# Kernel tuning notes

Measured on AMD Instinct MI355X. Metric: run time of the kernel, lower is better.

Reference implementation:

```python
import jax, jax.numpy as jnp
import numpy as np

B, S, D_MODEL, H = 4, 1024, 1024, 16
HD = D_MODEL // H  # head_dim = 64


def setup_inputs() -> dict:
    key = jax.random.key(0)
    ks = jax.random.split(key, 12)
    sd = 1.0 / np.sqrt(D_MODEL)
    return {
        "x": jax.random.normal(ks[0], (B, S, D_MODEL), dtype=jnp.float32),
        "Wq": jax.random.normal(ks[1], (D_MODEL, D_MODEL), dtype=jnp.float32) * sd,
        "bq": jnp.zeros((D_MODEL,), dtype=jnp.float32),
        "Wk": jax.random.normal(ks[2], (D_MODEL, D_MODEL), dtype=jnp.float32) * sd,
        "bk": jnp.zeros((D_MODEL,), dtype=jnp.float32),
        "Wv": jax.random.normal(ks[3], (D_MODEL, D_MODEL), dtype=jnp.float32) * sd,
        "bv": jnp.zeros((D_MODEL,), dtype=jnp.float32),
        "W1": jax.random.normal(ks[4], (2 * D_MODEL, D_MODEL), dtype=jnp.float32) * sd,
        "b1": jnp.zeros((2 * D_MODEL,), dtype=jnp.float32),
        "W2": jax.random.normal(ks[5], (D_MODEL, 2 * D_MODEL), dtype=jnp.float32) * (1.0 / np.sqrt(2 * D_MODEL)),
        "b2": jnp.zeros((D_MODEL,), dtype=jnp.float32),
        "mask": jnp.ones((B, S, S), dtype=jnp.int32),
    }


def reference(x, Wq, bq, Wk, bk, Wv, bv, W1, b1, W2, b2, mask):
    # QKV projections (torch Linear: y = x @ W.T + b), split into heads -> [B,H,S,HD]
    def proj(W, b):
        return (x @ W.T + b).reshape(B, S, H, HD).transpose(0, 2, 1, 3)

    q = proj(Wq, bq)
    k = proj(Wk, bk)
    v = proj(Wv, bv)

    scores = jnp.einsum("bhqd,bhkd->bhqk", q, k) / jnp.sqrt(jnp.float32(HD))
    # mask [B,S,S] broadcast over heads (original does unsqueeze(1).repeat)
    scores = jnp.where(mask[:, None, :, :] == 0, jnp.float32(-1e8), scores)
    probs = jax.nn.softmax(scores, axis=-1)
    ctx = jnp.einsum("bhqk,bhkd->bhqd", probs, v)
    ctx = ctx.transpose(0, 2, 1, 3).reshape(B, S, D_MODEL)

    # out-projection MLP: Linear(d, 2d) -> ReLU -> Linear(2d, d)
    h = jax.nn.relu(ctx @ W1.T + b1)
    return h @ W2.T + b2
```

## Files before the change

kernel.cpp:

```cpp
#include <hip/hip_runtime.h>
#include <hip/hip_bf16.h>
#include <stdint.h>


#define B_ 4
#define S_ 1024
#define DM_ 1024
#define H_ 16
#define HD_ 64

typedef __attribute__((ext_vector_type(8))) short short8;
typedef __attribute__((ext_vector_type(4))) float f32x4;
typedef __attribute__((ext_vector_type(4))) unsigned short ushort4v;

#define GLB_AS(p) ((const __attribute__((address_space(1))) void*)(p))
#define LDS_AS(p) ((__attribute__((address_space(3))) void*)(p))

__device__ __forceinline__ void async_load16(const void* g, void* l) {
  __builtin_amdgcn_global_load_lds(GLB_AS(g), LDS_AS(l), 16, 0, 0);
}

__device__ __forceinline__ unsigned short f2bf(float x) {
  union { float f; unsigned int u; } v; v.f = x;
  unsigned int r = v.u + 0x7fffu + ((v.u >> 16) & 1u);
  return (unsigned short)(r >> 16);
}

#define QSCALE 0.18033688011112042f

struct PrepArgs {
  const float* src[6];
  unsigned short* dst[6];
  int n4[6];
  const int* mask;
  unsigned long long* bits;
  unsigned int* rowflag;
  const float* bq;
  const float* bk;
  const float* bv;
  float* cb;
};

__global__ void prep_kernel(PrepArgs a) {
  const int seg = blockIdx.y;
  if (seg < 6) {
    const int n4 = a.n4[seg];
    const f32x4* __restrict__ src = (const f32x4*)a.src[seg];
    ushort4v* __restrict__ dst = (ushort4v*)a.dst[seg];
    for (int i = blockIdx.x * blockDim.x + threadIdx.x; i < n4;
         i += gridDim.x * blockDim.x) {
      f32x4 v = src[i];
      ushort4v o;
      o[0] = f2bf(v[0]); o[1] = f2bf(v[1]); o[2] = f2bf(v[2]); o[3] = f2bf(v[3]);
      dst[i] = o;
    }
  } else if (seg == 6) {
    const int wave = threadIdx.x >> 6;
    const int lane = threadIdx.x & 63;
    const int row = blockIdx.x * 4 + wave;
    const int4* mr = (const int4*)(a.mask + (size_t)row * S_) + lane * 4;
    unsigned int chunk = 0;
#pragma unroll
    for (int t = 0; t < 4; ++t) {
      const int4 v = mr[t];
      chunk |= (v.x != 0 ? 1u : 0u) << (4 * t + 0);
      chunk |= (v.y != 0 ? 1u : 0u) << (4 * t + 1);
      chunk |= (v.z != 0 ? 1u : 0u) << (4 * t + 2);
      chunk |= (v.w != 0 ? 1u : 0u) << (4 * t + 3);
    }
    unsigned long long v64 = (unsigned long long)chunk << (16 * (lane & 3));
    v64 |= __shfl_xor(v64, 1);
    v64 |= __shfl_xor(v64, 2);
    if ((lane & 3) == 0) a.bits[(size_t)row * 16 + (lane >> 2)] = v64;
    const bool all1 = (__ballot(chunk == 0xffffu) == ~0ull);
    if (lane == 0) a.rowflag[row] = all1 ? 1u : 0u;
  } else {
    const int i = blockIdx.x * 256 + threadIdx.x;
    if (i < 3072) {
      const float* src = (i < 1024) ? a.bq : (i < 2048) ? a.bk : a.bv;
      a.cb[i] = src[i & 1023];
    }
  }
}

enum { EPI_QKV = 0, EPI_RELU_BF16 = 2 };

template <int EPI>
__global__ __launch_bounds__(256, 3) void gemm_bt(
    const unsigned short* __restrict__ A, const unsigned short* __restrict__ Bt,
    const float* __restrict__ bias, void* __restrict__ Cp,
    unsigned short* __restrict__ Vt, int M, int N, int K, int Kld) {
  __shared__ __align__(16) unsigned short smem[128 * 136];
  unsigned short* sA = smem;
  unsigned short* sB = smem + 128 * 64;

  const int tid = threadIdx.x;
  const int lane = tid & 63;
  const int wave = tid >> 6;
  const int quad = lane >> 4;
  const int l15 = lane & 15;
  const int swzb = l15 & 7;
  const int m0 = blockIdx.y * 128;
  const int n0 = blockIdx.x * 128;
  const int wm = (wave >> 1) * 64;
  const int wn = (wave & 1) * 64;

  f32x4 acc[4][4];
#pragma unroll
  for (int i = 0; i < 4; ++i)
#pragma unroll
    for (int j = 0; j < 4; ++j) acc[i][j] = (f32x4){0.f, 0.f, 0.f, 0.f};

  const int srow = tid >> 3;
  const int scol = ((tid & 7) ^ (srow & 7)) * 8;
  const unsigned short* gA = A + (size_t)(m0 + srow) * Kld + scol;
  const unsigned short* gB = Bt + (size_t)(n0 + srow) * Kld + scol;
  unsigned short* lA = sA + tid * 8;
  unsigned short* lB = sB + tid * 8;

  for (int k0 = 0; k0 < K; k0 += 64) {
    __syncthreads();
#pragma unroll
    for (int st = 0; st < 4; ++st) {
      async_load16(gA + (size_t)(st * 32) * Kld + k0, lA + st * 2048);
      async_load16(gB + (size_t)(st * 32) * Kld + k0, lB + st * 2048);
    }
    __syncthreads();

#pragma unroll
    for (int ks = 0; ks < 2; ++ks) {
      short8 af[4], bfr[4];
#pragma unroll
      for (int t = 0; t < 4; ++t) {
        const int cg = ((ks * 4 + quad) ^ swzb) * 8;
        af[t] = *(const short8*)(sA + (wm + t * 16 + l15) * 64 + cg);
        bfr[t] = *(const short8*)(sB + (wn + t * 16 + l15) * 64 + cg);
      }
#pragma unroll
      for (int mt = 0; mt < 4; ++mt)
#pragma unroll
        for (int nt = 0; nt < 4; ++nt)
          acc[mt][nt] = __builtin_amdgcn_mfma_f32_16x16x32_bf16(
              af[mt], bfr[nt], acc[mt][nt], 0, 0, 0);
    }
  }

  if (EPI == EPI_QKV && n0 >= 2048) {
    __syncthreads();
#pragma unroll
    for (int nt = 0; nt < 4; ++nt) {
      const int col = n0 + wn + nt * 16 + l15;
      const float bv = bias[col];
#pragma unroll
      for (int mt = 0; mt < 4; ++mt)
#pragma unroll
        for (int r = 0; r < 4; ++r)
          smem[(wn + nt * 16 + l15) * 136 + wm + mt * 16 + quad * 4 + r] =
              f2bf(acc[mt][nt][r] + bv);
    }
    __syncthreads();
    const int vc0 = n0 - 2048;
    const int bb = m0 >> 10;
    const int s0 = m0 & 1023;
#pragma unroll
    for (int i = 0; i < 8; ++i) {
      const int c = i * 16 + (tid >> 4);
      const int tc = tid & 15;
      const short8 val = *(const short8*)(smem + c * 136 + tc * 8);
      const int ch = vc0 + c;
      const int hh = ch >> 6, dd = ch & 63;
      *(short8*)(Vt + ((size_t)(bb * 16 + hh) * HD_ + dd) * S_ + s0 + tc * 8) =
          val;
    }
    return;
  }

#pragma unroll
  for (int nt = 0; nt < 4; ++nt) {
    const int col = n0 + wn + nt * 16 + l15;
    const float bv = bias[col];
    const float scl = (EPI == EPI_QKV && col < 1024) ? QSCALE : 1.0f;
#pragma unroll
    for (int mt = 0; mt < 4; ++mt) {
#pragma unroll
      for (int r = 0; r < 4; ++r) {
        const int row = m0 + wm + mt * 16 + quad * 4 + r;
        float v = acc[mt][nt][r] + bv;
        if (EPI == EPI_RELU_BF16) {
          ((unsigned short*)Cp)[(size_t)row * N + col] = f2bf(fmaxf(v, 0.f));
        } else {
          ((unsigned short*)Cp)[(size_t)row * N + col] = f2bf(v * scl);
        }
      }
    }
  }
}

__global__ __launch_bounds__(512, 1) void gemm_ffn2(
    const unsigned short* __restrict__ A, const unsigned short* __restrict__ Bt,
    const float* __restrict__ bias, float* __restrict__ out) {
  __shared__ __align__(16) unsigned short smem[4 * 128 * 64];
  const int tid512 = threadIdx.x;
  const int half = tid512 >> 8;
  const int tid = tid512 & 255;
  unsigned short* sA = smem + half * 2 * 128 * 64;
  unsigned short* sB = sA + 128 * 64;

  const int lane = tid & 63;
  const int wave = tid >> 6;
  const int quad = lane >> 4;
  const int l15 = lane & 15;
  const int swzb = l15 & 7;
  const int m0 = blockIdx.y * 128;
  const int n0 = blockIdx.x * 128;
  const int wm = (wave >> 1) * 64;
  const int wn = (wave & 1) * 64;
  const int kz = half * 1024;

  f32x4 acc[4][4];
#pragma unroll
  for (int i = 0; i < 4; ++i)
#pragma unroll
    for (int j = 0; j < 4; ++j) acc[i][j] = (f32x4){0.f, 0.f, 0.f, 0.f};

  const int srow = tid >> 3;
  const int scol = ((tid & 7) ^ (srow & 7)) * 8;
  const unsigned short* gA = A + (size_t)(m0 + srow) * 2048 + kz + scol;
  const unsigned short* gB = Bt + (size_t)(n0 + srow) * 2048 + kz + scol;
  unsigned short* lA = sA + tid * 8;
  unsigned short* lB = sB + tid * 8;

  for (int k0 = 0; k0 < 1024; k0 += 64) {
    __syncthreads();
#pragma unroll
    for (int st = 0; st < 4; ++st) {
      async_load16(gA + (size_t)(st * 32) * 2048 + k0, lA + st * 2048);
      async_load16(gB + (size_t)(st * 32) * 2048 + k0, lB + st * 2048);
    }
    __syncthreads();

#pragma unroll
    for (int ks = 0; ks < 2; ++ks) {
      short8 af[4], bfr[4];
#pragma unroll
      for (int t = 0; t < 4; ++t) {
        const int cg = ((ks * 4 + quad) ^ swzb) * 8;
        af[t] = *(const short8*)(sA + (wm + t * 16 + l15) * 64 + cg);
        bfr[t] = *(const short8*)(sB + (wn + t * 16 + l15) * 64 + cg);
      }
#pragma unroll
      for (int mt = 0; mt < 4; ++mt)
#pragma unroll
        for (int nt = 0; nt < 4; ++nt)
          acc[mt][nt] = __builtin_amdgcn_mfma_f32_16x16x32_bf16(
              af[mt], bfr[nt], acc[mt][nt], 0, 0, 0);
    }
  }

  __syncthreads();
  float* fbuf = (float*)smem;
  if (half == 1) {
#pragma unroll
    for (int nt = 0; nt < 4; ++nt)
#pragma unroll
      for (int mt = 0; mt < 4; ++mt)
#pragma unroll
        for (int r = 0; r < 4; ++r)
          fbuf[wave * 4096 + (mt * 16 + quad * 4 + r) * 64 + nt * 16 + l15] =
              acc[mt][nt][r];
  }
  __syncthreads();
  if (half == 0) {
#pragma unroll
    for (int nt = 0; nt < 4; ++nt) {
      const int col = n0 + wn + nt * 16 + l15;
      const float bv = bias[col];
#pragma unroll
      for (int mt = 0; mt < 4; ++mt)
#pragma unroll
        for (int r = 0; r < 4; ++r) {
          const int row = m0 + wm + mt * 16 + quad * 4 + r;
          const float v =
              acc[mt][nt][r] +
              fbuf[wave * 4096 + (mt * 16 + quad * 4 + r) * 64 + nt * 16 + l15] +
              bv;
          out[(size_t)row * DM_ + col] = v;
        }
    }
  }
}

__global__ __launch_bounds__(256, 2) void flash_attn(
    const unsigned short* __restrict__ Cqkv, const unsigned short* __restrict__ Vt,
    const unsigned long long* __restrict__ mbits,
    const unsigned int* __restrict__ mrowflag,
    unsigned short* __restrict__ ctx) {
  __shared__ unsigned short sK[128 * 64];
  __shared__ unsigned short sV[64 * 128];
  __shared__ unsigned short spb[4][32 * 136];

  const int tid = threadIdx.x;
  const int wave = tid >> 6;
  const int lane = tid & 63;
  const int quad = lane >> 4;
  const int l15 = lane & 15;
  const int bh = blockIdx.x;
  const int b = bh >> 4;
  const int h = bh & 15;
  const int qbase = blockIdx.y * 128 + wave * 32;

  const unsigned short* Qb = Cqkv + (size_t)(b * S_) * 3072 + h * HD_;
  const unsigned short* Kb = Cqkv + (size_t)(b * S_) * 3072 + DM_ + h * HD_;
  const unsigned short* Vb = Vt + (size_t)bh * HD_ * S_;
  unsigned short* pbuf = spb[wave];

  bool mask_all_ones;
  {
    unsigned int f = mrowflag[b * S_ + qbase + (lane & 31)];
    mask_all_ones = (__ballot(f != 0) == ~0ull);
  }

  short8 qf[2][2];
#pragma unroll
  for (int u = 0; u < 2; ++u)
#pragma unroll
    for (int ks = 0; ks < 2; ++ks)
      qf[u][ks] = *(const short8*)(Qb + (size_t)(qbase + u * 16 + l15) * 3072 +
                                   ks * 32 + quad * 8);

  f32x4 o[2][4];
#pragma unroll
  for (int u = 0; u < 2; ++u)
#pragma unroll
    for (int i = 0; i < 4; ++i) o[u][i] = (f32x4){0.f, 0.f, 0.f, 0.f};
  float lsum[2][4] = {{0.f, 0.f, 0.f, 0.f}, {0.f, 0.f, 0.f, 0.f}};

  for (int kt = 0; kt < S_ / 128; ++kt) {
    const int kbase = kt * 128;

    __syncthreads();
#pragma unroll
    for (int st = 0; st < 4; ++st) {
      const int j = st * 256 + tid;
      const int r = j >> 3, c = j & 7;
      async_load16(Kb + (size_t)(kbase + r) * 3072 + ((c ^ (r & 7)) * 8),
                   sK + j * 8);
    }
#pragma unroll
    for (int st = 0; st < 4; ++st) {
      const int j = st * 256 + tid;
      const int d = j >> 4, c = j & 15;
      async_load16(Vb + (size_t)d * S_ + kbase + ((c ^ (d & 15)) * 8),
                   sV + j * 8);
    }
    __syncthreads();

    f32x4 s[2][8];
#pragma unroll
    for (int u = 0; u < 2; ++u)
#pragma unroll
      for (int i = 0; i < 8; ++i) s[u][i] = (f32x4){0.f, 0.f, 0.f, 0.f};
#pragma unroll
    for (int ks = 0; ks < 2; ++ks) {
      const int cg = ks * 4 + quad;
#pragma unroll
      for (int nt = 0; nt < 8; ++nt) {
        const int row = nt * 16 + l15;
        const short8 kf =
            *(const short8*)(sK + row * 64 + ((cg ^ (row & 7)) * 8));
        s[0][nt] = __builtin_amdgcn_mfma_f32_16x16x32_bf16(qf[0][ks], kf,
                                                           s[0][nt], 0, 0, 0);
        s[1][nt] = __builtin_amdgcn_mfma_f32_16x16x32_bf16(qf[1][ks], kf,
                                                           s[1][nt], 0, 0, 0);
      }
    }

    if (!mask_all_ones) {
#pragma unroll
      for (int u = 0; u < 2; ++u)
#pragma unroll
        for (int r = 0; r < 4; ++r) {
          const int q = qbase + u * 16 + quad * 4 + r;
          const unsigned long long* wp =
              mbits + ((size_t)(b * S_ + q)) * 16 + kt * 2;
          const unsigned long long w0 = wp[0], w1 = wp[1];
#pragma unroll
          for (int nt = 0; nt < 8; ++nt) {
            const unsigned long long w = (nt < 4) ? w0 : w1;
            const int bit = (nt * 16 + l15) & 63;
            if (!((w >> bit) & 1)) s[u][nt][r] = -1.0e8f;
          }
        }
    }

#pragma unroll
    for (int u = 0; u < 2; ++u)
#pragma unroll
      for (int nt = 0; nt < 8; ++nt)
#pragma unroll
        for (int r = 0; r < 4; ++r) {
          const float p = __builtin_amdgcn_exp2f(s[u][nt][r]);
          lsum[u][r] += p;
          pbuf[(u * 16 + quad * 4 + r) * 136 + nt * 16 + l15] = f2bf(p);
        }

#pragma unroll
    for (int ks2 = 0; ks2 < 4; ++ks2) {
      const short8 pf0 =
          *(const short8*)(pbuf + l15 * 136 + ks2 * 32 + quad * 8);
      const short8 pf1 =
          *(const short8*)(pbuf + (16 + l15) * 136 + ks2 * 32 + quad * 8);
      const int cg = ks2 * 4 + quad;
#pragma unroll
      for (int nt = 0; nt < 4; ++nt) {
        const int d = nt * 16 + l15;
        const short8 vf =
            *(const short8*)(sV + d * 128 + ((cg ^ (d & 15)) * 8));
        o[0][nt] = __builtin_amdgcn_mfma_f32_16x16x32_bf16(pf0, vf, o[0][nt], 0, 0, 0);
        o[1][nt] = __builtin_amdgcn_mfma_f32_16x16x32_bf16(pf1, vf, o[1][nt], 0, 0, 0);
      }
    }
  }

#pragma unroll
  for (int u = 0; u < 2; ++u)
#pragma unroll
    for (int r = 0; r < 4; ++r) {
      float lr = lsum[u][r];
      lr += __shfl_xor(lr, 1);
      lr += __shfl_xor(lr, 2);
      lr += __shfl_xor(lr, 4);
      lr += __shfl_xor(lr, 8);
      const float inv = 1.0f / lr;
#pragma unroll
      for (int nt = 0; nt < 4; ++nt)
        pbuf[(u * 16 + quad * 4 + r) * 68 + nt * 16 + l15] =
            f2bf(o[u][nt][r] * inv);
    }
#pragma unroll
  for (int i = 0; i < 4; ++i) {
    const int j = i * 64 + lane;
    const int r = j >> 3, c = j & 7;
    const short8 val = *(const short8*)(pbuf + r * 68 + c * 8);
    *(short8*)(ctx + ((size_t)b * S_ + qbase + r) * DM_ + h * HD_ + c * 8) = val;
  }
}

extern "C" void kernel_launch(void* const* d_in, const int* in_sizes, int n_in,
                              void* d_out, int out_size, void* d_ws,
                              size_t ws_size, hipStream_t stream) {
  const float* x = (const float*)d_in[0];
  const float* Wq = (const float*)d_in[1];
  const float* bq = (const float*)d_in[2];
  const float* Wk = (const float*)d_in[3];
  const float* bk = (const float*)d_in[4];
  const float* Wv = (const float*)d_in[5];
  const float* bv = (const float*)d_in[6];
  const float* W1 = (const float*)d_in[7];
  const float* b1 = (const float*)d_in[8];
  const float* W2 = (const float*)d_in[9];
  const float* b2 = (const float*)d_in[10];
  const int* mask = (const int*)d_in[11];
  float* out = (float*)d_out;

  char* ws = (char*)d_ws;
  unsigned short* xb   = (unsigned short*)(ws + 0);
  unsigned short* wqkv = (unsigned short*)(ws + 8388608);
  unsigned short* w1b  = (unsigned short*)(ws + 14680064);
  unsigned short* w2b  = (unsigned short*)(ws + 18874368);
  unsigned short* Cqkv = (unsigned short*)(ws + 23068672);
  unsigned short* ctxb = (unsigned short*)(ws + 48234496);
  unsigned short* hb   = (unsigned short*)(ws + 56623104);
  unsigned short* Vt   = (unsigned short*)(ws + 56623104);
  unsigned long long* mbits = (unsigned long long*)(ws + 73400320);
  unsigned int* mrowflag    = (unsigned int*)(ws + 73924608);
  float* cb                 = (float*)(ws + 73940992);

  PrepArgs pa;
  pa.src[0] = x;  pa.dst[0] = xb;               pa.n4[0] = (B_ * S_ * DM_) / 4;
  pa.src[1] = Wq; pa.dst[1] = wqkv;             pa.n4[1] = (DM_ * DM_) / 4;
  pa.src[2] = Wk; pa.dst[2] = wqkv + DM_ * DM_; pa.n4[2] = (DM_ * DM_) / 4;
  pa.src[3] = Wv; pa.dst[3] = wqkv + 2 * DM_ * DM_; pa.n4[3] = (DM_ * DM_) / 4;
  pa.src[4] = W1; pa.dst[4] = w1b;              pa.n4[4] = (2 * DM_ * DM_) / 4;
  pa.src[5] = W2; pa.dst[5] = w2b;              pa.n4[5] = (2 * DM_ * DM_) / 4;
  pa.mask = mask; pa.bits = mbits; pa.rowflag = mrowflag;
  pa.bq = bq; pa.bk = bk; pa.bv = bv; pa.cb = cb;
  prep_kernel<<<dim3(1024, 8), 256, 0, stream>>>(pa);

  const int M = B_ * S_;
  gemm_bt<EPI_QKV><<<dim3(3 * DM_ / 128, M / 128), 256, 0, stream>>>(
      xb, wqkv, cb, Cqkv, Vt, M, 3 * DM_, DM_, DM_);

  flash_attn<<<dim3(B_ * H_, S_ / 128), 256, 0, stream>>>(
      Cqkv, Vt, mbits, mrowflag, ctxb);

  gemm_bt<EPI_RELU_BF16><<<dim3((2 * DM_) / 128, M / 128), 256, 0, stream>>>(
      ctxb, w1b, b1, hb, nullptr, M, 2 * DM_, DM_, DM_);

  gemm_ffn2<<<dim3(DM_ / 128, M / 128), 512, 0, stream>>>(hb, w2b, b2, out);
}
```

Baseline: 231.2 us.

## Split attention over key halves with merge kernel; use intra-block split-K for FFN1

The flash-attention kernel now runs twice as many blocks, each covering half of the key range. It writes unnormalized fp32 partial outputs and row sums, and a new merge kernel adds the two halves, normalizes, and stores bf16 context. The FFN1 GEMM moves from the 256-thread gemm kernel to the templated 512-thread intra-block split-K kernel with a ReLU/bf16 epilogue, to get more waves per CU. The attention split adds an fp32 partial buffer round trip through global memory and an extra kernel launch.

New measurement: 248.5 us. 1.08x slower.

```diff
diff --git a/kernel.cpp b/kernel.cpp
--- a/kernel.cpp
+++ b/kernel.cpp
@@ -83,13 +83,10 @@
   }
 }
 
-enum { EPI_QKV = 0, EPI_RELU_BF16 = 2 };
-
-template <int EPI>
-__global__ __launch_bounds__(256, 3) void gemm_bt(
+__global__ __launch_bounds__(256, 3) void gemm_qkv(
     const unsigned short* __restrict__ A, const unsigned short* __restrict__ Bt,
-    const float* __restrict__ bias, void* __restrict__ Cp,
-    unsigned short* __restrict__ Vt, int M, int N, int K, int Kld) {
+    const float* __restrict__ bias, unsigned short* __restrict__ Cp,
+    unsigned short* __restrict__ Vt) {
   __shared__ __align__(16) unsigned short smem[128 * 136];
   unsigned short* sA = smem;
   unsigned short* sB = smem + 128 * 64;
@@ -104,6 +101,7 @@
   const int n0 = blockIdx.x * 128;
   const int wm = (wave >> 1) * 64;
   const int wn = (wave & 1) * 64;
+  const int N = 3 * DM_, Kld = DM_;
 
   f32x4 acc[4][4];
 #pragma unroll
@@ -118,7 +116,7 @@
   unsigned short* lA = sA + tid * 8;
   unsigned short* lB = sB + tid * 8;
 
-  for (int k0 = 0; k0 < K; k0 += 64) {
+  for (int k0 = 0; k0 < DM_; k0 += 64) {
     __syncthreads();
 #pragma unroll
     for (int st = 0; st < 4; ++st) {
@@ -145,7 +143,7 @@
     }
   }
 
-  if (EPI == EPI_QKV && n0 >= 2048) {
+  if (n0 >= 2048) {
     __syncthreads();
 #pragma unroll
     for (int nt = 0; nt < 4; ++nt) {
@@ -179,26 +177,21 @@
   for (int nt = 0; nt < 4; ++nt) {
     const int col = n0 + wn + nt * 16 + l15;
     const float bv = bias[col];
-    const float scl = (EPI == EPI_QKV && col < 1024) ? QSCALE : 1.0f;
-#pragma unroll
-    for (int mt = 0; mt < 4; ++mt) {
+    const float scl = (col < 1024) ? QSCALE : 1.0f;
+#pragma unroll
+    for (int mt = 0; mt < 4; ++mt)
 #pragma unroll
       for (int r = 0; r < 4; ++r) {
         const int row = m0 + wm + mt * 16 + quad * 4 + r;
-        float v = acc[mt][nt][r] + bv;
-        if (EPI == EPI_RELU_BF16) {
-          ((unsigned short*)Cp)[(size_t)row * N + col] = f2bf(fmaxf(v, 0.f));
-        } else {
-          ((unsigned short*)Cp)[(size_t)row * N + col] = f2bf(v * scl);
-        }
+        Cp[(size_t)row * N + col] = f2bf((acc[mt][nt][r] + bv) * scl);
       }
-    }
-  }
-}
-
-__global__ __launch_bounds__(512, 1) void gemm_ffn2(
+  }
+}
+
+template <int RELU>
+__global__ __launch_bounds__(512, 1) void gemm_splitk(
     const unsigned short* __restrict__ A, const unsigned short* __restrict__ Bt,
-    const float* __restrict__ bias, float* __restrict__ out) {
+    const float* __restrict__ bias, void* __restrict__ out, int N, int Kld) {
   __shared__ __align__(16) unsigned short smem[4 * 128 * 64];
   const int tid512 = threadIdx.x;
   const int half = tid512 >> 8;
@@ -215,7 +208,8 @@
   const int n0 = blockIdx.x * 128;
   const int wm = (wave >> 1) * 64;
   const int wn = (wave & 1) * 64;
-  const int kz = half * 1024;
+  const int Khalf = Kld >> 1;
+  const int kz = half * Khalf;
 
   f32x4 acc[4][4];
 #pragma unroll
@@ -225,17 +219,17 @@
 
   const int srow = tid >> 3;
   const int scol = ((tid & 7) ^ (srow & 7)) * 8;
-  const unsigned short* gA = A + (size_t)(m0 + srow) * 2048 + kz + scol;
-  const unsigned short* gB = Bt + (size_t)(n0 + srow) * 2048 + kz + scol;
+  const unsigned short* gA = A + (size_t)(m0 + srow) * Kld + kz + scol;
+  const unsigned short* gB = Bt + (size_t)(n0 + srow) * Kld + kz + scol;
   unsigned short* lA = sA + tid * 8;
   unsigned short* lB = sB + tid * 8;
 
-  for (int k0 = 0; k0 < 1024; k0 += 64) {
+  for (int k0 = 0; k0 < Khalf; k0 += 64) {
     __syncthreads();
 #pragma unroll
     for (int st = 0; st < 4; ++st) {
-      async_load16(gA + (size_t)(st * 32) * 2048 + k0, lA + st * 2048);
-      async_load16(gB + (size_t)(st * 32) * 2048 + k0, lB + st * 2048);
+      async_load16(gA + (size_t)(st * 32) * Kld + k0, lA + st * 2048);
+      async_load16(gB + (size_t)(st * 32) * Kld + k0, lB + st * 2048);
     }
     __syncthreads();
 
@@ -284,17 +278,20 @@
               acc[mt][nt][r] +
               fbuf[wave * 4096 + (mt * 16 + quad * 4 + r) * 64 + nt * 16 + l15] +
               bv;
-          out[(size_t)row * DM_ + col] = v;
+          if (RELU)
+            ((unsigned short*)out)[(size_t)row * N + col] = f2bf(fmaxf(v, 0.f));
+          else
+            ((float*)out)[(size_t)row * N + col] = v;
         }
     }
   }
 }
 
-__global__ __launch_bounds__(256, 2) void flash_attn(
+__global__ __launch_bounds__(256, 2) void flash_attn_split(
     const unsigned short* __restrict__ Cqkv, const unsigned short* __restrict__ Vt,
     const unsigned long long* __restrict__ mbits,
     const unsigned int* __restrict__ mrowflag,
-    unsigned short* __restrict__ ctx) {
+    float* __restrict__ Opart, float* __restrict__ lpart) {
   __shared__ unsigned short sK[128 * 64];
   __shared__ unsigned short sV[64 * 128];
   __shared__ unsigned short spb[4][32 * 136];
@@ -306,11 +303,12 @@
   const int l15 = lane & 15;
   const int bh = blockIdx.x;
   const int b = bh >> 4;
-  const int h = bh & 15;
+  const int kz = blockIdx.z;
   const int qbase = blockIdx.y * 128 + wave * 32;
 
-  const unsigned short* Qb = Cqkv + (size_t)(b * S_) * 3072 + h * HD_;
-  const unsigned short* Kb = Cqkv + (size_t)(b * S_) * 3072 + DM_ + h * HD_;
+  const unsigned short* Qb = Cqkv + (size_t)(b * S_) * 3072 + (bh & 15) * HD_;
+  const unsigned short* Kb =
+      Cqkv + (size_t)(b * S_) * 3072 + DM_ + (bh & 15) * HD_;
   const unsigned short* Vb = Vt + (size_t)bh * HD_ * S_;
   unsigned short* pbuf = spb[wave];
 
@@ -335,8 +333,9 @@
     for (int i = 0; i < 4; ++i) o[u][i] = (f32x4){0.f, 0.f, 0.f, 0.f};
   float lsum[2][4] = {{0.f, 0.f, 0.f, 0.f}, {0.f, 0.f, 0.f, 0.f}};
 
-  for (int kt = 0; kt < S_ / 128; ++kt) {
-    const int kbase = kt * 128;
+  for (int kt = 0; kt < 4; ++kt) {
+    const int ktile = kz * 4 + kt;
+    const int kbase = ktile * 128;
 
     __syncthreads();
 #pragma unroll
@@ -382,7 +381,7 @@
         for (int r = 0; r < 4; ++r) {
           const int q = qbase + u * 16 + quad * 4 + r;
           const unsigned long long* wp =
-              mbits + ((size_t)(b * S_ + q)) * 16 + kt * 2;
+              mbits + ((size_t)(b * S_ + q)) * 16 + ktile * 2;
           const unsigned long long w0 = wp[0], w1 = wp[1];
 #pragma unroll
           for (int nt = 0; nt < 8; ++nt) {
@@ -422,6 +421,7 @@
     }
   }
 
+  float* fb = (float*)pbuf;
 #pragma unroll
   for (int u = 0; u < 2; ++u)
 #pragma unroll
@@ -431,19 +431,42 @@
       lr += __shfl_xor(lr, 2);
       lr += __shfl_xor(lr, 4);
       lr += __shfl_xor(lr, 8);
-      const float inv = 1.0f / lr;
+      const int qrow = qbase + u * 16 + quad * 4 + r;
+      if (l15 == 0) lpart[((size_t)kz * 64 + bh) * S_ + qrow] = lr;
 #pragma unroll
       for (int nt = 0; nt < 4; ++nt)
-        pbuf[(u * 16 + quad * 4 + r) * 68 + nt * 16 + l15] =
-            f2bf(o[u][nt][r] * inv);
-    }
-#pragma unroll
-  for (int i = 0; i < 4; ++i) {
+        fb[(u * 16 + quad * 4 + r) * 68 + nt * 16 + l15] = o[u][nt][r];
+    }
+  float* obase = Opart + (((size_t)kz * 64 + bh) * S_ + qbase) * HD_;
+#pragma unroll
+  for (int i = 0; i < 8; ++i) {
     const int j = i * 64 + lane;
-    const int r = j >> 3, c = j & 7;
-    const short8 val = *(const short8*)(pbuf + r * 68 + c * 8);
-    *(short8*)(ctx + ((size_t)b * S_ + qbase + r) * DM_ + h * HD_ + c * 8) = val;
-  }
+    const int row = j >> 4, c = j & 15;
+    const f32x4 v = *(const f32x4*)(fb + row * 68 + c * 4);
+    *(f32x4*)(obase + (size_t)row * HD_ + c * 4) = v;
+  }
+}
+
+__global__ void merge_attn_kernel(const float* __restrict__ Opart,
+                                  const float* __restrict__ lpart,
+                                  unsigned short* __restrict__ ctx) {
+  const int bh = blockIdx.x;
+  const int b = bh >> 4, h = bh & 15;
+  const int row = threadIdx.x >> 4;
+  const int c = threadIdx.x & 15;
+  const int q = blockIdx.y * 16 + row;
+  const size_t base = ((size_t)bh * S_ + q) * HD_ + c * 4;
+  const f32x4 a0 = *(const f32x4*)(Opart + base);
+  const f32x4 a1 = *(const f32x4*)(Opart + (size_t)64 * S_ * HD_ + base);
+  const float l0 = lpart[(size_t)bh * S_ + q];
+  const float l1 = lpart[(size_t)64 * S_ + (size_t)bh * S_ + q];
+  const float inv = 1.0f / (l0 + l1);
+  ushort4v o;
+  o[0] = f2bf((a0[0] + a1[0]) * inv);
+  o[1] = f2bf((a0[1] + a1[1]) * inv);
+  o[2] = f2bf((a0[2] + a1[2]) * inv);
+  o[3] = f2bf((a0[3] + a1[3]) * inv);
+  *(ushort4v*)(ctx + ((size_t)b * S_ + q) * DM_ + h * HD_ + c * 4) = o;
 }
 
 extern "C" void kernel_launch(void* const* d_in, const int* in_sizes, int n_in,
@@ -475,6 +498,8 @@
   unsigned long long* mbits = (unsigned long long*)(ws + 73400320);
   unsigned int* mrowflag    = (unsigned int*)(ws + 73924608);
   float* cb                 = (float*)(ws + 73940992);
+  float* Opart = (float*)(ws + 83886080);
+  float* lpart = (float*)(ws + 117440512);
 
   PrepArgs pa;
   pa.src[0] = x;  pa.dst[0] = xb;               pa.n4[0] = (B_ * S_ * DM_) / 4;
@@ -488,14 +513,16 @@
   prep_kernel<<<dim3(1024, 8), 256, 0, stream>>>(pa);
 
   const int M = B_ * S_;
-  gemm_bt<EPI_QKV><<<dim3(3 * DM_ / 128, M / 128), 256, 0, stream>>>(
-      xb, wqkv, cb, Cqkv, Vt, M, 3 * DM_, DM_, DM_);
-
-  flash_attn<<<dim3(B_ * H_, S_ / 128), 256, 0, stream>>>(
-      Cqkv, Vt, mbits, mrowflag, ctxb);
-
-  gemm_bt<EPI_RELU_BF16><<<dim3((2 * DM_) / 128, M / 128), 256, 0, stream>>>(
-      ctxb, w1b, b1, hb, nullptr, M, 2 * DM_, DM_, DM_);
-
-  gemm_ffn2<<<dim3(DM_ / 128, M / 128), 512, 0, stream>>>(hb, w2b, b2, out);
-}
+  gemm_qkv<<<dim3(3 * DM_ / 128, M / 128), 256, 0, stream>>>(
+      xb, wqkv, cb, Cqkv, Vt);
+
+  flash_attn_split<<<dim3(B_ * H_, S_ / 128, 2), 256, 0, stream>>>(
+      Cqkv, Vt, mbits, mrowflag, Opart, lpart);
+  merge_attn_kernel<<<dim3(B_ * H_, S_ / 16), 256, 0, stream>>>(
+      Opart, lpart, ctxb);
+
+  gemm_splitk<1><<<dim3((2 * DM_) / 128, M / 128), 512, 0, stream>>>(
+      ctxb, w1b, b1, hb, 2 * DM_, DM_);
+  gemm_splitk<0><<<dim3(DM_ / 128, M / 128), 512, 0, stream>>>(
+      hb, w2b, b2, out, DM_, 2 * DM_);
+}
```
